# Kernel tuning notes

Hardware: AMD Instinct MI355X
Metric: run time of the kernel (lower is better)

Reference implementation:

```python
import jax, jax.numpy as jnp
import numpy as np

H = 128  # rnn_size

def _run_lstm(x, Wih, Whh, bih, bhh):
    # x: [B, T, D]; Wih: [4H, D]; Whh: [4H, H]; biases: [4H]
    B = x.shape[0]
    xg = jnp.einsum('btd,gd->btg', x, Wih) + bih + bhh  # precompute input projection [B,T,4H]
    WhhT = Whh.T  # [H, 4H]
    def step(carry, xg_t):
        h, c = carry
        g = xg_t + h @ WhhT  # [B, 4H]
        i = jax.nn.sigmoid(g[:, :H])
        f = jax.nn.sigmoid(g[:, H:2 * H])
        gg = jnp.tanh(g[:, 2 * H:3 * H])
        o = jax.nn.sigmoid(g[:, 3 * H:])
        c = f * c + i * gg
        h = o * jnp.tanh(c)
        return (h, c), h
    init = (jnp.zeros((B, H), x.dtype), jnp.zeros((B, H), x.dtype))
    _, ys = jax.lax.scan(step, init, jnp.swapaxes(xg, 0, 1))  # [T, B, H]
    return jnp.swapaxes(ys, 0, 1)  # [B, T, H]

def _bilstm(x, layers):
    h = x
    for (fw, bw) in layers:
        yf = _run_lstm(h, *fw)
        yb = jnp.flip(_run_lstm(jnp.flip(h, axis=1), *bw), axis=1)
        h = jnp.concatenate([yf, yb], axis=-1)  # [B, T, 2H]
    return h

def setup_inputs() -> dict:
    key = jax.random.key(0)
    ks = iter(jax.random.split(key, 32))
    B, T, D = 64, 512, 64
    s = 0.08  # init scale ~ 1/sqrt(H) to avoid gate saturation
    inp = {'x': jax.random.normal(next(ks), (B, T, D), jnp.float32)}
    for name, shape in [
        ('Wih00', (4 * H, D)), ('Whh00', (4 * H, H)), ('bih00', (4 * H,)), ('bhh00', (4 * H,)),
        ('Wih01', (4 * H, D)), ('Whh01', (4 * H, H)), ('bih01', (4 * H,)), ('bhh01', (4 * H,)),
        ('Wih10', (4 * H, 2 * H)), ('Whh10', (4 * H, H)), ('bih10', (4 * H,)), ('bhh10', (4 * H,)),
        ('Wih11', (4 * H, 2 * H)), ('Whh11', (4 * H, H)), ('bih11', (4 * H,)), ('bhh11', (4 * H,)),
        ('W1', (256, 2 * H)), ('b1', (256,)), ('W2', (D, 256)), ('b2', (D,)),
    ]:
        inp[name] = jax.random.normal(next(ks), shape, jnp.float32) * s
    return inp

def reference(x, Wih00, Whh00, bih00, bhh00, Wih01, Whh01, bih01, bhh01,
              Wih10, Whh10, bih10, bhh10, Wih11, Whh11, bih11, bhh11,
              W1, b1, W2, b2):
    layers = [((Wih00, Whh00, bih00, bhh00), (Wih01, Whh01, bih01, bhh01)),
              ((Wih10, Whh10, bih10, bhh10), (Wih11, Whh11, bih11, bhh11))]
    out = _bilstm(x, layers)  # [B, T, 2H]
    h = jax.nn.relu(jnp.einsum('bth,oh->bto', out, W1) + b1)
    return jnp.tanh(jnp.einsum('bth,oh->bto', h, W2) + b2)  # [B, T, input_size]
```

## Files before the change

kernel.cpp:

```cpp
#include <hip/hip_runtime.h>
#include <hip/hip_bf16.h>
#include <hip/hip_fp16.h>

typedef _Float16 h2vec __attribute__((ext_vector_type(2)));
typedef _Float16 f16x8 __attribute__((ext_vector_type(8)));
typedef float f32x4 __attribute__((ext_vector_type(4)));

static __device__ __forceinline__ float fast_sigmoid(float x) {
  return __builtin_amdgcn_rcpf(1.f + __expf(-x));
}
static __device__ __forceinline__ float fast_tanh(float x) {
  return 1.f - 2.f * __builtin_amdgcn_rcpf(__expf(2.f * x) + 1.f);
}
static __device__ __forceinline__ float fdot2u(unsigned int a, unsigned int b, float c) {
#if __has_builtin(__builtin_amdgcn_fdot2)
  return __builtin_amdgcn_fdot2(__builtin_bit_cast(h2vec, a),
                                __builtin_bit_cast(h2vec, b), c, false);
#else
  h2vec av = __builtin_bit_cast(h2vec, a);
  h2vec bv = __builtin_bit_cast(h2vec, b);
  return c + (float)av[0] * (float)bv[0] + (float)av[1] * (float)bv[1];
#endif
}
template<int CTRL>
static __device__ __forceinline__ float dpp_add(float v) {
  int x = __builtin_bit_cast(int, v);
  int y = __builtin_amdgcn_update_dpp(0, x, CTRL, 0xF, 0xF, true);
  return v + __builtin_bit_cast(float, y);
}
template<int CTRL>
static __device__ __forceinline__ float dpp_mov(float v) {
  int x = __builtin_bit_cast(int, v);
  int y = __builtin_amdgcn_update_dpp(0, x, CTRL, 0xF, 0xF, true);
  return __builtin_bit_cast(float, y);
}

template<typename AT>
static __device__ __forceinline__ void stage_row32(
    const AT* __restrict__ src, unsigned char* __restrict__ dst,
    int row, int kc ) {
#pragma unroll
  for (int u = 0; u < 4; ++u) {
    f16x8 h;
    if constexpr (sizeof(AT) == 4) {
      float4 v0 = *reinterpret_cast<const float4*>((const float*)src + u * 8);
      float4 v1 = *reinterpret_cast<const float4*>((const float*)src + u * 8 + 4);
      h[0] = (_Float16)v0.x; h[1] = (_Float16)v0.y;
      h[2] = (_Float16)v0.z; h[3] = (_Float16)v0.w;
      h[4] = (_Float16)v1.x; h[5] = (_Float16)v1.y;
      h[6] = (_Float16)v1.z; h[7] = (_Float16)v1.w;
    } else {
      h = *reinterpret_cast<const f16x8*>((const __half*)src + u * 8);
    }
    const int kbyte = (kc + u * 8) * 2;
    *reinterpret_cast<f16x8*>(&dst[row * 128 + (kbyte ^ ((row & 7) << 4))]) = h;
  }
}

template<typename AT, typename OT, int MODE>
__global__ __launch_bounds__(256) void gemm_mfma2(
    const AT* __restrict__ A, const float* __restrict__ W,
    const float* __restrict__ b0, const float* __restrict__ b1,
    OT* __restrict__ C, int M, int N, int K) {
  __shared__ __align__(16) unsigned char As[128 * 128];
  __shared__ __align__(16) unsigned char Bs[64 * 128];
  const int tid = threadIdx.x;
  const int wave = tid >> 6, l = tid & 63;
  const int wm = wave >> 1, wn = wave & 1;
  const int m0 = blockIdx.x * 128, n0 = blockIdx.y * 64;
  const int lrow = l & 15, lq = l >> 4;

  f32x4 acc[4][2] = {};
  const int arow = tid >> 1, akc = (tid & 1) * 32;
  const int brow = tid >> 2, bkc = (tid & 3) * 16;

  for (int k0 = 0; k0 < K; k0 += 64) {
    stage_row32<AT>(A + (size_t)(m0 + arow) * K + k0 + akc, As, arow, akc);
    {
      const float* src = W + (size_t)(n0 + brow) * K + k0 + bkc;
#pragma unroll
      for (int u = 0; u < 2; ++u) {
        float4 v0 = *reinterpret_cast<const float4*>(src + u * 8);
        float4 v1 = *reinterpret_cast<const float4*>(src + u * 8 + 4);
        f16x8 h;
        h[0] = (_Float16)v0.x; h[1] = (_Float16)v0.y;
        h[2] = (_Float16)v0.z; h[3] = (_Float16)v0.w;
        h[4] = (_Float16)v1.x; h[5] = (_Float16)v1.y;
        h[6] = (_Float16)v1.z; h[7] = (_Float16)v1.w;
        const int kbyte = (bkc + u * 8) * 2;
        *reinterpret_cast<f16x8*>(&Bs[brow * 128 + (kbyte ^ ((brow & 7) << 4))]) = h;
      }
    }
    __syncthreads();
#pragma unroll
    for (int kk = 0; kk < 64; kk += 32) {
      const int kbyte = (kk + lq * 8) * 2;
      f16x8 af[4], bf[2];
#pragma unroll
      for (int mt = 0; mt < 4; ++mt) {
        const int row = wm * 64 + mt * 16 + lrow;
        af[mt] = *reinterpret_cast<const f16x8*>(&As[row * 128 + (kbyte ^ ((row & 7) << 4))]);
      }
#pragma unroll
      for (int nt = 0; nt < 2; ++nt) {
        const int row = wn * 32 + nt * 16 + lrow;
        bf[nt] = *reinterpret_cast<const f16x8*>(&Bs[row * 128 + (kbyte ^ ((row & 7) << 4))]);
      }
#pragma unroll
      for (int mt = 0; mt < 4; ++mt)
#pragma unroll
        for (int nt = 0; nt < 2; ++nt)
          acc[mt][nt] = __builtin_amdgcn_mfma_f32_16x16x32_f16(af[mt], bf[nt], acc[mt][nt], 0, 0, 0);
    }
    __syncthreads();
  }

#pragma unroll
  for (int nt = 0; nt < 2; ++nt) {
    const int n = n0 + wn * 32 + nt * 16 + lrow;
    float bias = (MODE == 0) ? (b0[n] + b1[n]) : b0[n];
#pragma unroll
    for (int mt = 0; mt < 4; ++mt) {
#pragma unroll
      for (int r = 0; r < 4; ++r) {
        const int m = m0 + wm * 64 + mt * 16 + lq * 4 + r;
        float val = acc[mt][nt][r] + bias;
        if (MODE == 1) val = fmaxf(val, 0.f);
        if (MODE == 2) val = fast_tanh(val);
        if constexpr (sizeof(OT) == 2)
          C[(size_t)m * N + n] = __float2half_rn(val);
        else
          C[(size_t)m * N + n] = val;
      }
    }
  }
}

template<typename AT>
__global__ __launch_bounds__(256) void gemm_proj_h(
    const AT* __restrict__ A,
    const float* __restrict__ W0, const float* __restrict__ W1,
    const float* __restrict__ bi0, const float* __restrict__ bh0,
    const float* __restrict__ bi1, const float* __restrict__ bh1,
    __half* __restrict__ C0, __half* __restrict__ C1, int M, int N, int K) {
  const float* __restrict__ W  = blockIdx.z ? W1 : W0;
  const float* __restrict__ b0 = blockIdx.z ? bi1 : bi0;
  const float* __restrict__ b1 = blockIdx.z ? bh1 : bh0;
  __half* __restrict__ C = blockIdx.z ? C1 : C0;

  __shared__ __align__(16) unsigned char As[128 * 128];
  __shared__ __align__(16) unsigned char Bs[64 * 128];
  const int tid = threadIdx.x;
  const int wave = tid >> 6, l = tid & 63;
  const int wm = wave >> 1, wn = wave & 1;
  const int m0 = blockIdx.x * 128, n0 = blockIdx.y * 64;
  const int lrow = l & 15, lq = l >> 4;

  f32x4 acc[4][2] = {};
  const int arow = tid >> 1, akc = (tid & 1) * 32;
  const int brow = tid >> 2, bkc = (tid & 3) * 16;

  for (int k0 = 0; k0 < K; k0 += 64) {
    stage_row32<AT>(A + (size_t)(m0 + arow) * K + k0 + akc, As, arow, akc);
    {
      const float* src = W + (size_t)(n0 + brow) * K + k0 + bkc;
#pragma unroll
      for (int u = 0; u < 2; ++u) {
        float4 v0 = *reinterpret_cast<const float4*>(src + u * 8);
        float4 v1 = *reinterpret_cast<const float4*>(src + u * 8 + 4);
        f16x8 h;
        h[0] = (_Float16)v0.x; h[1] = (_Float16)v0.y;
        h[2] = (_Float16)v0.z; h[3] = (_Float16)v0.w;
        h[4] = (_Float16)v1.x; h[5] = (_Float16)v1.y;
        h[6] = (_Float16)v1.z; h[7] = (_Float16)v1.w;
        const int kbyte = (bkc + u * 8) * 2;
        *reinterpret_cast<f16x8*>(&Bs[brow * 128 + (kbyte ^ ((brow & 7) << 4))]) = h;
      }
    }
    __syncthreads();
#pragma unroll
    for (int kk = 0; kk < 64; kk += 32) {
      const int kbyte = (kk + lq * 8) * 2;
      f16x8 af[4], bf[2];
#pragma unroll
      for (int mt = 0; mt < 4; ++mt) {
        const int row = wm * 64 + mt * 16 + lrow;
        af[mt] = *reinterpret_cast<const f16x8*>(&As[row * 128 + (kbyte ^ ((row & 7) << 4))]);
      }
#pragma unroll
      for (int nt = 0; nt < 2; ++nt) {
        const int row = wn * 32 + nt * 16 + lrow;
        bf[nt] = *reinterpret_cast<const f16x8*>(&Bs[row * 128 + (kbyte ^ ((row & 7) << 4))]);
      }
#pragma unroll
      for (int mt = 0; mt < 4; ++mt)
#pragma unroll
        for (int nt = 0; nt < 2; ++nt)
          acc[mt][nt] = __builtin_amdgcn_mfma_f32_16x16x32_f16(af[mt], bf[nt], acc[mt][nt], 0, 0, 0);
    }
    __syncthreads();
  }

#pragma unroll
  for (int nt = 0; nt < 2; ++nt) {
    const int n = n0 + wn * 32 + nt * 16 + lrow;
    const float bias = b0[n] + b1[n];
#pragma unroll
    for (int mt = 0; mt < 4; ++mt) {
#pragma unroll
      for (int r = 0; r < 4; ++r) {
        const int m = m0 + wm * 64 + mt * 16 + lq * 4 + r;
        C[(size_t)m * N + n] = __float2half_rn(acc[mt][nt][r] + bias);
      }
    }
  }
}

__global__ __launch_bounds__(512, 2) void lstm_seq5h(
    const __half* __restrict__ xg_f, const __half* __restrict__ xg_b,
    const float* __restrict__ Whh_f, const float* __restrict__ Whh_b,
    __half* __restrict__ out) {
  const int b = blockIdx.x;
  const int dir = blockIdx.y;
  const int tid = threadIdx.x;
  const int j = tid >> 2;
  const int kq = tid & 3;
  const __half* __restrict__ xg = dir ? xg_b : xg_f;
  const float* __restrict__ Whh = dir ? Whh_b : Whh_f;

  __shared__ unsigned int hbuf[2][64];

  unsigned int w[4][16];
#pragma unroll
  for (int g = 0; g < 4; ++g) {
    const float4* wr = reinterpret_cast<const float4*>(
        Whh + (size_t)(g * 128 + j) * 128 + kq * 32);
#pragma unroll
    for (int q = 0; q < 8; ++q) {
      float4 v = wr[q];
      __half2 p0 = __floats2half2_rn(v.x, v.y);
      __half2 p1 = __floats2half2_rn(v.z, v.w);
      w[g][2 * q]     = __builtin_bit_cast(unsigned int, p0);
      w[g][2 * q + 1] = __builtin_bit_cast(unsigned int, p1);
    }
  }

  if (tid < 128) hbuf[tid >> 6][tid & 63] = 0u;
  float c = 0.f;
  __syncthreads();

  const int tt0 = dir ? 511 : 0;
  const int stp = dir ? -1 : 1;
  const size_t base = (size_t)b * 512 * 512;
  const int xidx = kq * 128 + j;

  unsigned short xva = __builtin_bit_cast(unsigned short, xg[base + (size_t)tt0 * 512 + xidx]);
  unsigned short xvb = __builtin_bit_cast(unsigned short, xg[base + (size_t)(tt0 + stp) * 512 + xidx]);

  auto step = [&](int t, unsigned int* rbuf, unsigned int* wbuf, unsigned short& xcur)
      __attribute__((always_inline)) {
    const int tt = tt0 + stp * t;

    const uint4* hc = reinterpret_cast<const uint4*>(&rbuf[kq * 16]);
    uint4 q0 = hc[0], q1 = hc[1], q2 = hc[2], q3 = hc[3];
    unsigned int ha[16];
    ha[0] = q0.x; ha[1] = q0.y; ha[2] = q0.z; ha[3] = q0.w;
    ha[4] = q1.x; ha[5] = q1.y; ha[6] = q1.z; ha[7] = q1.w;
    ha[8] = q2.x; ha[9] = q2.y; ha[10] = q2.z; ha[11] = q2.w;
    ha[12] = q3.x; ha[13] = q3.y; ha[14] = q3.z; ha[15] = q3.w;

    float acc[4] = {0.f, 0.f, 0.f, 0.f};
#pragma unroll
    for (int kk = 0; kk < 16; ++kk) {
#pragma unroll
      for (int g = 0; g < 4; ++g)
        acc[g] = fdot2u(w[g][kk], ha[kk], acc[g]);
    }

#pragma unroll
    for (int g = 0; g < 4; ++g) {
      float a = acc[g];
      a = dpp_add<0xB1>(a);
      a = dpp_add<0x4E>(a);
      acc[g] = a;
    }

    float a = acc[0];
    a = (kq == 1) ? acc[1] : a;
    a = (kq == 2) ? acc[2] : a;
    a = (kq == 3) ? acc[3] : a;
    a += (float)__builtin_bit_cast(_Float16, xcur);

    {
      const int t2 = t + 2;
      const int tt2 = (t2 < 512) ? (tt0 + stp * t2) : tt0;
      xcur = __builtin_bit_cast(unsigned short, xg[base + (size_t)tt2 * 512 + xidx]);
    }

    const float xs = (kq == 2) ? 2.f * a : a;
    const float y = fast_sigmoid(xs);
    const float act = (kq == 2) ? 2.f * y - 1.f : y;

    const float gi = dpp_mov<0x00>(act);
    const float gf = dpp_mov<0x55>(act);
    const float gg = dpp_mov<0xAA>(act);
    const float go = dpp_mov<0xFF>(act);

    c = gf * c + gi * gg;
    const float h = go * (2.f * fast_sigmoid(2.f * c) - 1.f);

    if (kq == 0) {
      unsigned short us = __builtin_bit_cast(unsigned short, (_Float16)h);
      reinterpret_cast<unsigned short*>(wbuf)[j] = us;
    }
    if (kq == 1) {
      out[((size_t)b * 512 + tt) * 256 + dir * 128 + j] = __float2half_rn(h);
    }

    asm volatile("s_waitcnt lgkmcnt(0)" ::: "memory");
    __builtin_amdgcn_s_barrier();
    asm volatile("" ::: "memory");
  };

  for (int it = 0; it < 256; ++it) {
    step(2 * it,     hbuf[0], hbuf[1], xva);
    step(2 * it + 1, hbuf[1], hbuf[0], xvb);
  }
}

extern "C" void kernel_launch(void* const* d_in, const int* in_sizes, int n_in,
                              void* d_out, int out_size, void* d_ws, size_t ws_size,
                              hipStream_t stream) {
  (void)in_sizes; (void)n_in; (void)out_size; (void)ws_size;

  const float* x     = (const float*)d_in[0];
  const float* Wih00 = (const float*)d_in[1];
  const float* Whh00 = (const float*)d_in[2];
  const float* bih00 = (const float*)d_in[3];
  const float* bhh00 = (const float*)d_in[4];
  const float* Wih01 = (const float*)d_in[5];
  const float* Whh01 = (const float*)d_in[6];
  const float* bih01 = (const float*)d_in[7];
  const float* bhh01 = (const float*)d_in[8];
  const float* Wih10 = (const float*)d_in[9];
  const float* Whh10 = (const float*)d_in[10];
  const float* bih10 = (const float*)d_in[11];
  const float* bhh10 = (const float*)d_in[12];
  const float* Wih11 = (const float*)d_in[13];
  const float* Whh11 = (const float*)d_in[14];
  const float* bih11 = (const float*)d_in[15];
  const float* bhh11 = (const float*)d_in[16];
  const float* W1 = (const float*)d_in[17];
  const float* b1 = (const float*)d_in[18];
  const float* W2 = (const float*)d_in[19];
  const float* b2 = (const float*)d_in[20];
  float* out = (float*)d_out;

  char* ws = (char*)d_ws;
  __half* xgh_f = (__half*)ws;
  __half* xgh_b = (__half*)(ws + ((size_t)32 << 20));
  __half* bufh  = (__half*)(ws + ((size_t)64 << 20));
  __half* tmph  = (__half*)(ws + ((size_t)80 << 20));

  const int M = 64 * 512;

  gemm_proj_h<float><<<dim3(M / 128, 8, 2), 256, 0, stream>>>(
      x, Wih00, Wih01, bih00, bhh00, bih01, bhh01, xgh_f, xgh_b, M, 512, 64);
  lstm_seq5h<<<dim3(64, 2), 512, 0, stream>>>(xgh_f, xgh_b, Whh00, Whh01, bufh);

  gemm_proj_h<__half><<<dim3(M / 128, 8, 2), 256, 0, stream>>>(
      bufh, Wih10, Wih11, bih10, bhh10, bih11, bhh11, xgh_f, xgh_b, M, 512, 256);
  lstm_seq5h<<<dim3(64, 2), 512, 0, stream>>>(xgh_f, xgh_b, Whh10, Whh11, bufh);

  gemm_mfma2<__half, __half, 1><<<dim3(M / 128, 4), 256, 0, stream>>>(
      bufh, W1, b1, nullptr, tmph, M, 256, 256);
  gemm_mfma2<__half, float, 2><<<dim3(M / 128, 1), 256, 0, stream>>>(
      tmph, W2, b2, nullptr, out, M, 64, 256);
}
```

Baseline: 629.9 us.

## Halve LSTM recurrence block size by computing two hidden units per thread

The recurrent LSTM kernel now runs 256 threads per block instead of 512, and each thread-quad handles two adjacent hidden units. Each thread holds twice the recurrent weights in registers (128 packed fp16 pairs), and input-gate and output values move as packed half2 words. Fewer waves share each per-step barrier, which should cut synchronisation cost and give more independent FMA chains per thread. The trade-off is higher register pressure and twice the serial dot-product work per thread on the critical path.

New measurement: 788.6 us. +25.2%, slower.

```diff
diff --git a/kernel.cpp b/kernel.cpp
--- a/kernel.cpp
+++ b/kernel.cpp
@@ -38,7 +38,7 @@
 template<typename AT>
 static __device__ __forceinline__ void stage_row32(
     const AT* __restrict__ src, unsigned char* __restrict__ dst,
-    int row, int kc ) {
+    int row, int kc) {
 #pragma unroll
   for (int u = 0; u < 4; ++u) {
     f16x8 h;
@@ -216,48 +216,50 @@
   }
 }
 
-__global__ __launch_bounds__(512, 2) void lstm_seq5h(
+__global__ __launch_bounds__(256, 1) void lstm_seq8(
     const __half* __restrict__ xg_f, const __half* __restrict__ xg_b,
     const float* __restrict__ Whh_f, const float* __restrict__ Whh_b,
     __half* __restrict__ out) {
   const int b = blockIdx.x;
   const int dir = blockIdx.y;
   const int tid = threadIdx.x;
-  const int j = tid >> 2;
+  const int j2 = tid >> 2;
   const int kq = tid & 3;
   const __half* __restrict__ xg = dir ? xg_b : xg_f;
   const float* __restrict__ Whh = dir ? Whh_b : Whh_f;
 
   __shared__ unsigned int hbuf[2][64];
 
-  unsigned int w[4][16];
-#pragma unroll
-  for (int g = 0; g < 4; ++g) {
-    const float4* wr = reinterpret_cast<const float4*>(
-        Whh + (size_t)(g * 128 + j) * 128 + kq * 32);
-#pragma unroll
-    for (int q = 0; q < 8; ++q) {
-      float4 v = wr[q];
-      __half2 p0 = __floats2half2_rn(v.x, v.y);
-      __half2 p1 = __floats2half2_rn(v.z, v.w);
-      w[g][2 * q]     = __builtin_bit_cast(unsigned int, p0);
-      w[g][2 * q + 1] = __builtin_bit_cast(unsigned int, p1);
-    }
-  }
+  unsigned int w[4][2][16];
+#pragma unroll
+  for (int g = 0; g < 4; ++g)
+#pragma unroll
+    for (int u = 0; u < 2; ++u) {
+      const float4* wr = reinterpret_cast<const float4*>(
+          Whh + (size_t)(g * 128 + 2 * j2 + u) * 128 + kq * 32);
+#pragma unroll
+      for (int q = 0; q < 8; ++q) {
+        float4 v = wr[q];
+        __half2 p0 = __floats2half2_rn(v.x, v.y);
+        __half2 p1 = __floats2half2_rn(v.z, v.w);
+        w[g][u][2 * q]     = __builtin_bit_cast(unsigned int, p0);
+        w[g][u][2 * q + 1] = __builtin_bit_cast(unsigned int, p1);
+      }
+    }
 
   if (tid < 128) hbuf[tid >> 6][tid & 63] = 0u;
-  float c = 0.f;
+  float c0 = 0.f, c1 = 0.f;
   __syncthreads();
 
   const int tt0 = dir ? 511 : 0;
   const int stp = dir ? -1 : 1;
   const size_t base = (size_t)b * 512 * 512;
-  const int xidx = kq * 128 + j;
-
-  unsigned short xva = __builtin_bit_cast(unsigned short, xg[base + (size_t)tt0 * 512 + xidx]);
-  unsigned short xvb = __builtin_bit_cast(unsigned short, xg[base + (size_t)(tt0 + stp) * 512 + xidx]);
-
-  auto step = [&](int t, unsigned int* rbuf, unsigned int* wbuf, unsigned short& xcur)
+  const int xoff = kq * 128 + 2 * j2;
+
+  unsigned int xva = *reinterpret_cast<const unsigned int*>(xg + base + (size_t)tt0 * 512 + xoff);
+  unsigned int xvb = *reinterpret_cast<const unsigned int*>(xg + base + (size_t)(tt0 + stp) * 512 + xoff);
+
+  auto step = [&](int t, unsigned int* rbuf, unsigned int* wbuf, unsigned int& xcur)
       __attribute__((always_inline)) {
     const int tt = tt0 + stp * t;
 
@@ -269,52 +271,63 @@
     ha[8] = q2.x; ha[9] = q2.y; ha[10] = q2.z; ha[11] = q2.w;
     ha[12] = q3.x; ha[13] = q3.y; ha[14] = q3.z; ha[15] = q3.w;
 
-    float acc[4] = {0.f, 0.f, 0.f, 0.f};
+    float acc[4][2] = {};
 #pragma unroll
     for (int kk = 0; kk < 16; ++kk) {
 #pragma unroll
-      for (int g = 0; g < 4; ++g)
-        acc[g] = fdot2u(w[g][kk], ha[kk], acc[g]);
-    }
-
-#pragma unroll
-    for (int g = 0; g < 4; ++g) {
-      float a = acc[g];
-      a = dpp_add<0xB1>(a);
-      a = dpp_add<0x4E>(a);
-      acc[g] = a;
-    }
-
-    float a = acc[0];
-    a = (kq == 1) ? acc[1] : a;
-    a = (kq == 2) ? acc[2] : a;
-    a = (kq == 3) ? acc[3] : a;
-    a += (float)__builtin_bit_cast(_Float16, xcur);
-
+      for (int g = 0; g < 4; ++g) {
+        acc[g][0] = fdot2u(w[g][0][kk], ha[kk], acc[g][0]);
+        acc[g][1] = fdot2u(w[g][1][kk], ha[kk], acc[g][1]);
+      }
+    }
+
+#pragma unroll
+    for (int g = 0; g < 4; ++g)
+#pragma unroll
+      for (int u = 0; u < 2; ++u) {
+        float a = acc[g][u];
+        a = dpp_add<0xB1>(a);
+        a = dpp_add<0x4E>(a);
+        acc[g][u] = a;
+      }
+
+    const __half2 xh = __builtin_bit_cast(__half2, xcur);
     {
       const int t2 = t + 2;
       const int tt2 = (t2 < 512) ? (tt0 + stp * t2) : tt0;
-      xcur = __builtin_bit_cast(unsigned short, xg[base + (size_t)tt2 * 512 + xidx]);
-    }
-
-    const float xs = (kq == 2) ? 2.f * a : a;
-    const float y = fast_sigmoid(xs);
-    const float act = (kq == 2) ? 2.f * y - 1.f : y;
-
-    const float gi = dpp_mov<0x00>(act);
-    const float gf = dpp_mov<0x55>(act);
-    const float gg = dpp_mov<0xAA>(act);
-    const float go = dpp_mov<0xFF>(act);
-
-    c = gf * c + gi * gg;
-    const float h = go * (2.f * fast_sigmoid(2.f * c) - 1.f);
-
+      xcur = *reinterpret_cast<const unsigned int*>(xg + base + (size_t)tt2 * 512 + xoff);
+    }
+
+    float h01[2];
+#pragma unroll
+    for (int u = 0; u < 2; ++u) {
+      float a = acc[0][u];
+      a = (kq == 1) ? acc[1][u] : a;
+      a = (kq == 2) ? acc[2][u] : a;
+      a = (kq == 3) ? acc[3][u] : a;
+      a += (u == 0) ? __low2float(xh) : __high2float(xh);
+
+      const float xs = (kq == 2) ? 2.f * a : a;
+      const float y = fast_sigmoid(xs);
+      const float act = (kq == 2) ? 2.f * y - 1.f : y;
+
+      const float gi = dpp_mov<0x00>(act);
+      const float gf = dpp_mov<0x55>(act);
+      const float gg = dpp_mov<0xAA>(act);
+      const float go = dpp_mov<0xFF>(act);
+
+      float& c = (u == 0) ? c0 : c1;
+      c = gf * c + gi * gg;
+      h01[u] = go * (2.f * fast_sigmoid(2.f * c) - 1.f);
+    }
+
+    const __half2 hp = __floats2half2_rn(h01[0], h01[1]);
     if (kq == 0) {
-      unsigned short us = __builtin_bit_cast(unsigned short, (_Float16)h);
-      reinterpret_cast<unsigned short*>(wbuf)[j] = us;
+      wbuf[j2] = __builtin_bit_cast(unsigned int, hp);
     }
     if (kq == 1) {
-      out[((size_t)b * 512 + tt) * 256 + dir * 128 + j] = __float2half_rn(h);
+      *reinterpret_cast<__half2*>(
+          out + ((size_t)b * 512 + tt) * 256 + dir * 128 + 2 * j2) = hp;
     }
 
     asm volatile("s_waitcnt lgkmcnt(0)" ::: "memory");
@@ -366,11 +379,11 @@
 
   gemm_proj_h<float><<<dim3(M / 128, 8, 2), 256, 0, stream>>>(
       x, Wih00, Wih01, bih00, bhh00, bih01, bhh01, xgh_f, xgh_b, M, 512, 64);
-  lstm_seq5h<<<dim3(64, 2), 512, 0, stream>>>(xgh_f, xgh_b, Whh00, Whh01, bufh);
+  lstm_seq8<<<dim3(64, 2), 256, 0, stream>>>(xgh_f, xgh_b, Whh00, Whh01, bufh);
 
   gemm_proj_h<__half><<<dim3(M / 128, 8, 2), 256, 0, stream>>>(
       bufh, Wih10, Wih11, bih10, bhh10, bih11, bhh11, xgh_f, xgh_b, M, 512, 256);
-  lstm_seq5h<<<dim3(64, 2), 512, 0, stream>>>(xgh_f, xgh_b, Whh10, Whh11, bufh);
+  lstm_seq8<<<dim3(64, 2), 256, 0, stream>>>(xgh_f, xgh_b, Whh10, Whh11, bufh);
 
   gemm_mfma2<__half, __half, 1><<<dim3(M / 128, 4), 256, 0, stream>>>(
       bufh, W1, b1, nullptr, tmph, M, 256, 256);
```

## Fuse forward and backward LSTM directions into one block per batch row

Applied to the files above, without the earlier changes.

The recurrent kernel now runs both directions inside a single 512-thread block per batch element, holding both directions' recurrent weights in registers and interleaving their dot products, activations and state updates. This halves the grid to 64 blocks and shares one barrier per timestep between the two independent chains, exposing more instruction-level parallelism per wave to hide latency. In exchange it doubles register pressure (128 weight registers per thread), which may force spills or lower occupancy, and uses fewer CUs on a 256-CU device.

After: 1.043 ms. 65.6% more time.

```diff
diff --git a/kernel.cpp b/kernel.cpp
--- a/kernel.cpp
+++ b/kernel.cpp
@@ -38,7 +38,7 @@
 template<typename AT>
 static __device__ __forceinline__ void stage_row32(
     const AT* __restrict__ src, unsigned char* __restrict__ dst,
-    int row, int kc ) {
+    int row, int kc) {
 #pragma unroll
   for (int u = 0; u < 4; ++u) {
     f16x8 h;
@@ -216,105 +216,138 @@
   }
 }
 
-__global__ __launch_bounds__(512, 2) void lstm_seq5h(
+__global__ __launch_bounds__(512, 2) void lstm_dual(
     const __half* __restrict__ xg_f, const __half* __restrict__ xg_b,
     const float* __restrict__ Whh_f, const float* __restrict__ Whh_b,
     __half* __restrict__ out) {
   const int b = blockIdx.x;
-  const int dir = blockIdx.y;
   const int tid = threadIdx.x;
   const int j = tid >> 2;
   const int kq = tid & 3;
-  const __half* __restrict__ xg = dir ? xg_b : xg_f;
-  const float* __restrict__ Whh = dir ? Whh_b : Whh_f;
-
-  __shared__ unsigned int hbuf[2][64];
-
-  unsigned int w[4][16];
+
+  __shared__ unsigned int hbuf[2][2][64];
+
+  unsigned int wa[4][16], wb[4][16];
 #pragma unroll
   for (int g = 0; g < 4; ++g) {
-    const float4* wr = reinterpret_cast<const float4*>(
-        Whh + (size_t)(g * 128 + j) * 128 + kq * 32);
+    const float4* wrA = reinterpret_cast<const float4*>(
+        Whh_f + (size_t)(g * 128 + j) * 128 + kq * 32);
+    const float4* wrB = reinterpret_cast<const float4*>(
+        Whh_b + (size_t)(g * 128 + j) * 128 + kq * 32);
 #pragma unroll
     for (int q = 0; q < 8; ++q) {
-      float4 v = wr[q];
-      __half2 p0 = __floats2half2_rn(v.x, v.y);
-      __half2 p1 = __floats2half2_rn(v.z, v.w);
-      w[g][2 * q]     = __builtin_bit_cast(unsigned int, p0);
-      w[g][2 * q + 1] = __builtin_bit_cast(unsigned int, p1);
-    }
-  }
-
-  if (tid < 128) hbuf[tid >> 6][tid & 63] = 0u;
-  float c = 0.f;
+      float4 va = wrA[q];
+      float4 vb = wrB[q];
+      wa[g][2 * q]     = __builtin_bit_cast(unsigned int, __floats2half2_rn(va.x, va.y));
+      wa[g][2 * q + 1] = __builtin_bit_cast(unsigned int, __floats2half2_rn(va.z, va.w));
+      wb[g][2 * q]     = __builtin_bit_cast(unsigned int, __floats2half2_rn(vb.x, vb.y));
+      wb[g][2 * q + 1] = __builtin_bit_cast(unsigned int, __floats2half2_rn(vb.z, vb.w));
+    }
+  }
+
+  if (tid < 256) reinterpret_cast<unsigned int*>(hbuf)[tid] = 0u;
+  float ca = 0.f, cb = 0.f;
   __syncthreads();
 
-  const int tt0 = dir ? 511 : 0;
-  const int stp = dir ? -1 : 1;
   const size_t base = (size_t)b * 512 * 512;
   const int xidx = kq * 128 + j;
 
-  unsigned short xva = __builtin_bit_cast(unsigned short, xg[base + (size_t)tt0 * 512 + xidx]);
-  unsigned short xvb = __builtin_bit_cast(unsigned short, xg[base + (size_t)(tt0 + stp) * 512 + xidx]);
-
-  auto step = [&](int t, unsigned int* rbuf, unsigned int* wbuf, unsigned short& xcur)
+  unsigned short xaA = __builtin_bit_cast(unsigned short, xg_f[base + (size_t)0 * 512 + xidx]);
+  unsigned short xbA = __builtin_bit_cast(unsigned short, xg_f[base + (size_t)1 * 512 + xidx]);
+  unsigned short xaB = __builtin_bit_cast(unsigned short, xg_b[base + (size_t)511 * 512 + xidx]);
+  unsigned short xbB = __builtin_bit_cast(unsigned short, xg_b[base + (size_t)510 * 512 + xidx]);
+
+  auto step = [&](int t, unsigned int* rA, unsigned int* wA_,
+                  unsigned int* rB, unsigned int* wB_,
+                  unsigned short& xcA, unsigned short& xcB)
       __attribute__((always_inline)) {
-    const int tt = tt0 + stp * t;
-
-    const uint4* hc = reinterpret_cast<const uint4*>(&rbuf[kq * 16]);
-    uint4 q0 = hc[0], q1 = hc[1], q2 = hc[2], q3 = hc[3];
-    unsigned int ha[16];
-    ha[0] = q0.x; ha[1] = q0.y; ha[2] = q0.z; ha[3] = q0.w;
-    ha[4] = q1.x; ha[5] = q1.y; ha[6] = q1.z; ha[7] = q1.w;
-    ha[8] = q2.x; ha[9] = q2.y; ha[10] = q2.z; ha[11] = q2.w;
-    ha[12] = q3.x; ha[13] = q3.y; ha[14] = q3.z; ha[15] = q3.w;
-
-    float acc[4] = {0.f, 0.f, 0.f, 0.f};
-#pragma unroll
-    for (int kk = 0; kk < 16; ++kk) {
-#pragma unroll
-      for (int g = 0; g < 4; ++g)
-        acc[g] = fdot2u(w[g][kk], ha[kk], acc[g]);
-    }
-
-#pragma unroll
-    for (int g = 0; g < 4; ++g) {
-      float a = acc[g];
-      a = dpp_add<0xB1>(a);
-      a = dpp_add<0x4E>(a);
-      acc[g] = a;
-    }
-
-    float a = acc[0];
-    a = (kq == 1) ? acc[1] : a;
-    a = (kq == 2) ? acc[2] : a;
-    a = (kq == 3) ? acc[3] : a;
-    a += (float)__builtin_bit_cast(_Float16, xcur);
+    const int ttA = t;
+    const int ttB = 511 - t;
+
+    const uint4* hcA = reinterpret_cast<const uint4*>(&rA[kq * 16]);
+    const uint4* hcB = reinterpret_cast<const uint4*>(&rB[kq * 16]);
+    const uint4 qA0 = hcA[0], qA1 = hcA[1], qA2 = hcA[2], qA3 = hcA[3];
+    const uint4 qB0 = hcB[0], qB1 = hcB[1], qB2 = hcB[2], qB3 = hcB[3];
+
+    float aA0 = 0.f, aA1 = 0.f, aA2 = 0.f, aA3 = 0.f;
+    float aB0 = 0.f, aB1 = 0.f, aB2 = 0.f, aB3 = 0.f;
+#define ACC2(kk, hA, hB)                     \
+    aA0 = fdot2u(wa[0][kk], (hA), aA0);      \
+    aB0 = fdot2u(wb[0][kk], (hB), aB0);      \
+    aA1 = fdot2u(wa[1][kk], (hA), aA1);      \
+    aB1 = fdot2u(wb[1][kk], (hB), aB1);      \
+    aA2 = fdot2u(wa[2][kk], (hA), aA2);      \
+    aB2 = fdot2u(wb[2][kk], (hB), aB2);      \
+    aA3 = fdot2u(wa[3][kk], (hA), aA3);      \
+    aB3 = fdot2u(wb[3][kk], (hB), aB3);
+    ACC2(0,  qA0.x, qB0.x) ACC2(1,  qA0.y, qB0.y)
+    ACC2(2,  qA0.z, qB0.z) ACC2(3,  qA0.w, qB0.w)
+    ACC2(4,  qA1.x, qB1.x) ACC2(5,  qA1.y, qB1.y)
+    ACC2(6,  qA1.z, qB1.z) ACC2(7,  qA1.w, qB1.w)
+    ACC2(8,  qA2.x, qB2.x) ACC2(9,  qA2.y, qB2.y)
+    ACC2(10, qA2.z, qB2.z) ACC2(11, qA2.w, qB2.w)
+    ACC2(12, qA3.x, qB3.x) ACC2(13, qA3.y, qB3.y)
+    ACC2(14, qA3.z, qB3.z) ACC2(15, qA3.w, qB3.w)
+#undef ACC2
+
+    aA0 = dpp_add<0x4E>(dpp_add<0xB1>(aA0));
+    aB0 = dpp_add<0x4E>(dpp_add<0xB1>(aB0));
+    aA1 = dpp_add<0x4E>(dpp_add<0xB1>(aA1));
+    aB1 = dpp_add<0x4E>(dpp_add<0xB1>(aB1));
+    aA2 = dpp_add<0x4E>(dpp_add<0xB1>(aA2));
+    aB2 = dpp_add<0x4E>(dpp_add<0xB1>(aB2));
+    aA3 = dpp_add<0x4E>(dpp_add<0xB1>(aA3));
+    aB3 = dpp_add<0x4E>(dpp_add<0xB1>(aB3));
+
+    float sA = aA0;
+    sA = (kq == 1) ? aA1 : sA;
+    sA = (kq == 2) ? aA2 : sA;
+    sA = (kq == 3) ? aA3 : sA;
+    sA += (float)__builtin_bit_cast(_Float16, xcA);
+    float sB = aB0;
+    sB = (kq == 1) ? aB1 : sB;
+    sB = (kq == 2) ? aB2 : sB;
+    sB = (kq == 3) ? aB3 : sB;
+    sB += (float)__builtin_bit_cast(_Float16, xcB);
 
     {
       const int t2 = t + 2;
-      const int tt2 = (t2 < 512) ? (tt0 + stp * t2) : tt0;
-      xcur = __builtin_bit_cast(unsigned short, xg[base + (size_t)tt2 * 512 + xidx]);
-    }
-
-    const float xs = (kq == 2) ? 2.f * a : a;
-    const float y = fast_sigmoid(xs);
-    const float act = (kq == 2) ? 2.f * y - 1.f : y;
-
-    const float gi = dpp_mov<0x00>(act);
-    const float gf = dpp_mov<0x55>(act);
-    const float gg = dpp_mov<0xAA>(act);
-    const float go = dpp_mov<0xFF>(act);
-
-    c = gf * c + gi * gg;
-    const float h = go * (2.f * fast_sigmoid(2.f * c) - 1.f);
+      const int tA2 = (t2 < 512) ? t2 : 0;
+      const int tB2 = (t2 < 512) ? (511 - t2) : 511;
+      xcA = __builtin_bit_cast(unsigned short, xg_f[base + (size_t)tA2 * 512 + xidx]);
+      xcB = __builtin_bit_cast(unsigned short, xg_b[base + (size_t)tB2 * 512 + xidx]);
+    }
+
+    const float xsA = (kq == 2) ? 2.f * sA : sA;
+    const float xsB = (kq == 2) ? 2.f * sB : sB;
+    const float yA = fast_sigmoid(xsA);
+    const float yB = fast_sigmoid(xsB);
+    const float actA = (kq == 2) ? 2.f * yA - 1.f : yA;
+    const float actB = (kq == 2) ? 2.f * yB - 1.f : yB;
+
+    const float giA = dpp_mov<0x00>(actA);
+    const float giB = dpp_mov<0x00>(actB);
+    const float gfA = dpp_mov<0x55>(actA);
+    const float gfB = dpp_mov<0x55>(actB);
+    const float ggA = dpp_mov<0xAA>(actA);
+    const float ggB = dpp_mov<0xAA>(actB);
+    const float goA = dpp_mov<0xFF>(actA);
+    const float goB = dpp_mov<0xFF>(actB);
+
+    ca = gfA * ca + giA * ggA;
+    cb = gfB * cb + giB * ggB;
+    const float hA = goA * (2.f * fast_sigmoid(2.f * ca) - 1.f);
+    const float hB = goB * (2.f * fast_sigmoid(2.f * cb) - 1.f);
 
     if (kq == 0) {
-      unsigned short us = __builtin_bit_cast(unsigned short, (_Float16)h);
-      reinterpret_cast<unsigned short*>(wbuf)[j] = us;
+      reinterpret_cast<unsigned short*>(wA_)[j] =
+          __builtin_bit_cast(unsigned short, (_Float16)hA);
+      reinterpret_cast<unsigned short*>(wB_)[j] =
+          __builtin_bit_cast(unsigned short, (_Float16)hB);
     }
     if (kq == 1) {
-      out[((size_t)b * 512 + tt) * 256 + dir * 128 + j] = __float2half_rn(h);
+      out[((size_t)b * 512 + ttA) * 256 + j] = __float2half_rn(hA);
+      out[((size_t)b * 512 + ttB) * 256 + 128 + j] = __float2half_rn(hB);
     }
 
     asm volatile("s_waitcnt lgkmcnt(0)" ::: "memory");
@@ -323,8 +356,8 @@
   };
 
   for (int it = 0; it < 256; ++it) {
-    step(2 * it,     hbuf[0], hbuf[1], xva);
-    step(2 * it + 1, hbuf[1], hbuf[0], xvb);
+    step(2 * it,     hbuf[0][0], hbuf[0][1], hbuf[1][0], hbuf[1][1], xaA, xaB);
+    step(2 * it + 1, hbuf[0][1], hbuf[0][0], hbuf[1][1], hbuf[1][0], xbA, xbB);
   }
 }
 
@@ -366,11 +399,11 @@
 
   gemm_proj_h<float><<<dim3(M / 128, 8, 2), 256, 0, stream>>>(
       x, Wih00, Wih01, bih00, bhh00, bih01, bhh01, xgh_f, xgh_b, M, 512, 64);
-  lstm_seq5h<<<dim3(64, 2), 512, 0, stream>>>(xgh_f, xgh_b, Whh00, Whh01, bufh);
+  lstm_dual<<<dim3(64), 512, 0, stream>>>(xgh_f, xgh_b, Whh00, Whh01, bufh);
 
   gemm_proj_h<__half><<<dim3(M / 128, 8, 2), 256, 0, stream>>>(
       bufh, Wih10, Wih11, bih10, bhh10, bih11, bhh11, xgh_f, xgh_b, M, 512, 256);
-  lstm_seq5h<<<dim3(64, 2), 512, 0, stream>>>(xgh_f, xgh_b, Whh10, Whh11, bufh);
+  lstm_dual<<<dim3(64), 512, 0, stream>>>(xgh_f, xgh_b, Whh10, Whh11, bufh);
 
   gemm_mfma2<__half, __half, 1><<<dim3(M / 128, 4), 256, 0, stream>>>(
       bufh, W1, b1, nullptr, tmph, M, 256, 256);
```
